# Optimization experiments

Hardware: AMD Instinct MI355X
Metric: run time of the kernel (lower is better)

The kernel has to match this reference:

```python
import jax, jax.numpy as jnp
import numpy as np

NUM_HEADS = 16

def setup_inputs() -> dict:
    B, S, H = 2, 2048, 1024
    Hh = H // 2
    key = jax.random.key(0)
    ks = jax.random.split(key, 16)
    sd = 1.0 / np.sqrt(H)
    sdh = 1.0 / np.sqrt(Hh)
    return {
        "query": jax.random.normal(ks[0], (B, S, H), jnp.float32),
        "key_in": jax.random.normal(ks[1], (B, S, H), jnp.float32),
        "value": jax.random.normal(ks[2], (B, S, H), jnp.float32),
        "direction_signal": jax.random.randint(ks[3], (B, S), 0, 3, jnp.int64),
        # Linear weights stored as (in, out); y = x @ W + b (same math as torch x @ W.T + b)
        "Wq_w": jax.random.normal(ks[4], (H, H), jnp.float32) * sd,
        "Wq_b": jnp.zeros((H,), jnp.float32),
        "Wk_w": jax.random.normal(ks[5], (H, H), jnp.float32) * sd,
        "Wk_b": jnp.zeros((H,), jnp.float32),
        "Wv_w": jax.random.normal(ks[6], (H, H), jnp.float32) * sd,
        "Wv_b": jnp.zeros((H,), jnp.float32),
        "ds1_w": jax.random.normal(ks[7], (H, Hh), jnp.float32) * sd,
        "ds1_b": jnp.zeros((Hh,), jnp.float32),
        "ds2_w": jax.random.normal(ks[8], (Hh, NUM_HEADS), jnp.float32) * sdh,
        "ds2_b": jnp.zeros((NUM_HEADS,), jnp.float32),
        "fo_w": jax.random.normal(ks[9], (H, H), jnp.float32) * sd,
        "fo_b": jnp.zeros((H,), jnp.float32),
    }

def reference(query, key_in, value, direction_signal,
              Wq_w, Wq_b, Wk_w, Wk_b, Wv_w, Wv_b,
              ds1_w, ds1_b, ds2_w, ds2_b, fo_w, fo_b):
    B, S, H = query.shape
    nh = NUM_HEADS
    hd = H // nh
    scale = np.sqrt(hd).astype(np.float32)

    def split_heads(x):  # (B,S,H) -> (B,nh,S,hd)
        return x.reshape(B, S, nh, hd).transpose(0, 2, 1, 3)

    Q = split_heads(query @ Wq_w + Wq_b)
    K = split_heads(key_in @ Wk_w + Wk_b)
    V = split_heads(value @ Wv_w + Wv_b)

    scores = jnp.einsum('bhqd,bhkd->bhqk', Q, K) / scale

    # direction bias: per-(batch, head, query) additive scalar broadcast over keys
    # torch nn.GELU default is exact (erf) -> approximate=False
    dir_w = jax.nn.gelu(query @ ds1_w + ds1_b, approximate=False) @ ds2_w + ds2_b  # (B,S,nh)
    scores = scores + 0.3 * dir_w.transpose(0, 2, 1)[..., None]

    attention = jax.nn.softmax(scores, axis=-1)
    # dropout is identity in eval/reference mode
    context = jnp.einsum('bhqk,bhkd->bqhd', attention, V).reshape(B, S, H)
    output = context @ fo_w + fo_b
    return output, attention
```

## Files before the change

kernel.cpp:

```cpp
#include <hip/hip_runtime.h>


typedef unsigned short u16;
typedef unsigned int   u32;
typedef _Float16       f16;
typedef f16   half8   __attribute__((ext_vector_type(8)));
typedef float floatx4 __attribute__((ext_vector_type(4)));
typedef u32   u32x4   __attribute__((ext_vector_type(4)));

union V8 { u16 u[8]; u32x4 v; };

__device__ __forceinline__ u16 f16_bits(float f){
    union { f16 h; u16 u; } x; x.h = (f16)f; return x.u;
}

template<typename TI>
__global__ __launch_bounds__(256) void transpose_k(
    const TI* __restrict__ in, u16* __restrict__ out,
    long irs, long ors, int zdiv, long ibs0, long ibs1, long obs0, long obs1)
{
    __shared__ u16 tile[64][72];
    int z = blockIdx.z;
    const TI* ip = in  + (long)(z / zdiv) * ibs0 + (long)(z % zdiv) * ibs1;
    u16*      op = out + (long)(z / zdiv) * obs0 + (long)(z % zdiv) * obs1;
    long r0 = (long)blockIdx.y * 64, c0 = (long)blockIdx.x * 64;
    int t = threadIdx.x;
    int r = t >> 2, cs = (t & 3) * 16;
#pragma unroll
    for (int j = 0; j < 16; j++){
        TI v = ip[(r0 + r) * irs + c0 + cs + j];
        if (sizeof(TI) == 4) tile[r][cs + j] = f16_bits((float)v);
        else                 tile[r][cs + j] = (u16)v;
    }
    __syncthreads();
#pragma unroll
    for (int j = 0; j < 16; j++){
        op[(c0 + r) * ors + r0 + cs + j] = tile[cs + j][r];
    }
}

__global__ __launch_bounds__(256) void transpose_w4(
    const float* __restrict__ w0, const float* __restrict__ w1,
    const float* __restrict__ w2, const float* __restrict__ w3,
    u16* __restrict__ o0, u16* __restrict__ o1,
    u16* __restrict__ o2, u16* __restrict__ o3)
{
    __shared__ u16 tile[64][72];
    int z = blockIdx.z;
    const float* ip = (z == 0) ? w0 : (z == 1) ? w1 : (z == 2) ? w2 : w3;
    u16*         op = (z == 0) ? o0 : (z == 1) ? o1 : (z == 2) ? o2 : o3;
    long r0 = (long)blockIdx.y * 64, c0 = (long)blockIdx.x * 64;
    int t = threadIdx.x;
    int r = t >> 2, cs = (t & 3) * 16;
#pragma unroll
    for (int j = 0; j < 16; j++)
        tile[r][cs + j] = f16_bits(ip[(r0 + r) * 1024 + c0 + cs + j]);
    __syncthreads();
#pragma unroll
    for (int j = 0; j < 16; j++)
        op[(c0 + r) * 1024 + r0 + cs + j] = tile[cs + j][r];
}

template<bool A_F32, bool OUT_F32>
__global__ __launch_bounds__(256) void gemm_bt(
    const void* __restrict__ Av, const u16* __restrict__ BT,
    const float* __restrict__ bias, void* __restrict__ Cv,
    int M, int N, int K, float out_scale)
{
    __shared__ u16 Alds[64][40];
    __shared__ u16 Blds[64][40];
    int m0 = blockIdx.y * 64, n0 = blockIdx.x * 64;
    int t = threadIdx.x, w = t >> 6, lane = t & 63, quad = lane >> 4, l16 = lane & 15;
    int wm = (w >> 1) * 32, wn = (w & 1) * 32;
    const floatx4 zero4 = {0.f, 0.f, 0.f, 0.f};
    floatx4 acc[2][2];
#pragma unroll
    for (int i = 0; i < 2; i++)
#pragma unroll
        for (int j = 0; j < 2; j++) acc[i][j] = zero4;

    int srow = t >> 2, scol = (t & 3) * 8;
    const float* Apf = (const float*)Av + (long)(m0 + srow) * K + scol;
    const u16*   Aph = (const u16*)Av   + (long)(m0 + srow) * K + scol;
    const u16*   Bp  = BT + (long)(n0 + srow) * K + scol;

    for (int k0 = 0; k0 < K; k0 += 32){
        __syncthreads();
        V8 va, vb;
        if (A_F32){
            floatx4 a0 = *(const floatx4*)(Apf + k0);
            floatx4 a1 = *(const floatx4*)(Apf + k0 + 4);
#pragma unroll
            for (int j = 0; j < 4; j++){
                va.u[j]     = f16_bits(a0[j]);
                va.u[4 + j] = f16_bits(a1[j]);
            }
        } else {
            va.v = *(const u32x4*)(Aph + k0);
        }
        vb.v = *(const u32x4*)(Bp + k0);
        *(u32x4*)&Alds[srow][scol] = va.v;
        *(u32x4*)&Blds[srow][scol] = vb.v;
        __syncthreads();
        half8 a0 = *(const half8*)&Alds[wm + l16][quad * 8];
        half8 a1 = *(const half8*)&Alds[wm + 16 + l16][quad * 8];
        half8 b0 = *(const half8*)&Blds[wn + l16][quad * 8];
        half8 b1 = *(const half8*)&Blds[wn + 16 + l16][quad * 8];
        acc[0][0] = __builtin_amdgcn_mfma_f32_16x16x32_f16(a0, b0, acc[0][0], 0, 0, 0);
        acc[0][1] = __builtin_amdgcn_mfma_f32_16x16x32_f16(a0, b1, acc[0][1], 0, 0, 0);
        acc[1][0] = __builtin_amdgcn_mfma_f32_16x16x32_f16(a1, b0, acc[1][0], 0, 0, 0);
        acc[1][1] = __builtin_amdgcn_mfma_f32_16x16x32_f16(a1, b1, acc[1][1], 0, 0, 0);
    }

#pragma unroll
    for (int mi = 0; mi < 2; mi++)
#pragma unroll
        for (int ni = 0; ni < 2; ni++){
            int n = n0 + wn + ni * 16 + l16;
            float bv = bias[n];
#pragma unroll
            for (int r = 0; r < 4; r++){
                int m = m0 + wm + mi * 16 + quad * 4 + r;
                float v = (acc[mi][ni][r] + bv) * out_scale;
                if (OUT_F32) ((float*)Cv)[(long)m * N + n] = v;
                else         ((u16*)Cv)[(long)m * N + n]   = f16_bits(v);
            }
        }
}

__global__ __launch_bounds__(256) void gemm_qkv(
    const float* __restrict__ Aq, const float* __restrict__ Ak, const float* __restrict__ Avv,
    const u16* __restrict__ Bq, const u16* __restrict__ Bk, const u16* __restrict__ Bv,
    const float* __restrict__ bq, const float* __restrict__ bk, const float* __restrict__ bv,
    u16* __restrict__ Cq, u16* __restrict__ Ck, u16* __restrict__ Cv,
    int M, int N, int K)
{
    __shared__ u16 Alds[64][40];
    __shared__ u16 Blds[64][40];
    int z = blockIdx.z;
    const float* A    = (z == 0) ? Aq : (z == 1) ? Ak : Avv;
    const u16*   BT   = (z == 0) ? Bq : (z == 1) ? Bk : Bv;
    const float* bias = (z == 0) ? bq : (z == 1) ? bk : bv;
    u16*         C    = (z == 0) ? Cq : (z == 1) ? Ck : Cv;
    float out_scale   = (z == 0) ? 0.125f : 1.0f;

    int m0 = blockIdx.y * 64, n0 = blockIdx.x * 64;
    int t = threadIdx.x, w = t >> 6, lane = t & 63, quad = lane >> 4, l16 = lane & 15;
    int wm = (w >> 1) * 32, wn = (w & 1) * 32;
    const floatx4 zero4 = {0.f, 0.f, 0.f, 0.f};
    floatx4 acc[2][2];
#pragma unroll
    for (int i = 0; i < 2; i++)
#pragma unroll
        for (int j = 0; j < 2; j++) acc[i][j] = zero4;

    int srow = t >> 2, scol = (t & 3) * 8;
    const float* Apf = A + (long)(m0 + srow) * K + scol;
    const u16*   Bp  = BT + (long)(n0 + srow) * K + scol;

    for (int k0 = 0; k0 < K; k0 += 32){
        __syncthreads();
        V8 va, vb;
        floatx4 a0 = *(const floatx4*)(Apf + k0);
        floatx4 a1 = *(const floatx4*)(Apf + k0 + 4);
#pragma unroll
        for (int j = 0; j < 4; j++){
            va.u[j]     = f16_bits(a0[j]);
            va.u[4 + j] = f16_bits(a1[j]);
        }
        vb.v = *(const u32x4*)(Bp + k0);
        *(u32x4*)&Alds[srow][scol] = va.v;
        *(u32x4*)&Blds[srow][scol] = vb.v;
        __syncthreads();
        half8 af0 = *(const half8*)&Alds[wm + l16][quad * 8];
        half8 af1 = *(const half8*)&Alds[wm + 16 + l16][quad * 8];
        half8 bf0 = *(const half8*)&Blds[wn + l16][quad * 8];
        half8 bf1 = *(const half8*)&Blds[wn + 16 + l16][quad * 8];
        acc[0][0] = __builtin_amdgcn_mfma_f32_16x16x32_f16(af0, bf0, acc[0][0], 0, 0, 0);
        acc[0][1] = __builtin_amdgcn_mfma_f32_16x16x32_f16(af0, bf1, acc[0][1], 0, 0, 0);
        acc[1][0] = __builtin_amdgcn_mfma_f32_16x16x32_f16(af1, bf0, acc[1][0], 0, 0, 0);
        acc[1][1] = __builtin_amdgcn_mfma_f32_16x16x32_f16(af1, bf1, acc[1][1], 0, 0, 0);
    }

#pragma unroll
    for (int mi = 0; mi < 2; mi++)
#pragma unroll
        for (int ni = 0; ni < 2; ni++){
            int n = n0 + wn + ni * 16 + l16;
            float bv = bias[n];
#pragma unroll
            for (int r = 0; r < 4; r++){
                int m = m0 + wm + mi * 16 + quad * 4 + r;
                C[(long)m * N + n] = f16_bits((acc[mi][ni][r] + bv) * out_scale);
            }
        }
}

#define S_LEN 2048
#define NH 16
#define HD 64

__global__ __launch_bounds__(256, 4) void attn_k(
    const u16* __restrict__ Q, const u16* __restrict__ K,
    const u16* __restrict__ VT, float* __restrict__ attn,
    u16* __restrict__ ctx)
{
    __shared__ u16 Plds[64][72];
    int bx0 = blockIdx.x;
    int bx = ((bx0 & 7) << 7) | (bx0 >> 3);
    int qb = bx & 31, h = (bx >> 5) & 15, b = bx >> 9;
    int q0 = qb * 64;
    int t = threadIdx.x, w = t >> 6, lane = t & 63, quad = lane >> 4, l16 = lane & 15;
    const u16* Qp  = Q + (long)b * S_LEN * 1024 + h * HD;
    const u16* Kp  = K + (long)b * S_LEN * 1024 + h * HD;
    const u16* VTp = VT + ((long)(b * NH + h)) * HD * S_LEN;

    int qrow = q0 + w * 16 + l16;
    half8 qf0 = *(const half8*)(Qp + (long)qrow * 1024 + quad * 8);
    half8 qf1 = *(const half8*)(Qp + (long)qrow * 1024 + 32 + quad * 8);

    const floatx4 zero4 = {0.f, 0.f, 0.f, 0.f};
    float lsum[4] = {0.f, 0.f, 0.f, 0.f};

    for (int k0 = 0; k0 < S_LEN; k0 += 64){
        floatx4 sc[4];
#pragma unroll
        for (int kt = 0; kt < 4; kt++){
            const u16* kr = Kp + (long)(k0 + kt * 16 + l16) * 1024;
            half8 kf0 = *(const half8*)(kr + quad * 8);
            half8 kf1 = *(const half8*)(kr + 32 + quad * 8);
            sc[kt] = __builtin_amdgcn_mfma_f32_16x16x32_f16(qf0, kf0, zero4, 0, 0, 0);
            sc[kt] = __builtin_amdgcn_mfma_f32_16x16x32_f16(qf1, kf1, sc[kt], 0, 0, 0);
        }
#pragma unroll
        for (int kt = 0; kt < 4; kt++)
#pragma unroll
            for (int r = 0; r < 4; r++) lsum[r] += __expf(sc[kt][r]);
    }
    float linv[4];
#pragma unroll
    for (int r = 0; r < 4; r++){
        float s = lsum[r];
#pragma unroll
        for (int off = 1; off < 16; off <<= 1) s += __shfl_xor(s, off);
        linv[r] = 1.f / s;
    }

    floatx4 ctxa[4];
#pragma unroll
    for (int dt = 0; dt < 4; dt++) ctxa[dt] = zero4;

    long arow0 = ((long)(b * NH + h) * S_LEN + (q0 + w * 16 + quad * 4)) * S_LEN;

    for (int k0 = 0; k0 < S_LEN; k0 += 64){
        floatx4 sc[4];
#pragma unroll
        for (int kt = 0; kt < 4; kt++){
            const u16* kr = Kp + (long)(k0 + kt * 16 + l16) * 1024;
            half8 kf0 = *(const half8*)(kr + quad * 8);
            half8 kf1 = *(const half8*)(kr + 32 + quad * 8);
            sc[kt] = __builtin_amdgcn_mfma_f32_16x16x32_f16(qf0, kf0, zero4, 0, 0, 0);
            sc[kt] = __builtin_amdgcn_mfma_f32_16x16x32_f16(qf1, kf1, sc[kt], 0, 0, 0);
        }
#pragma unroll
        for (int kt = 0; kt < 4; kt++)
#pragma unroll
            for (int r = 0; r < 4; r++){
                float p = __expf(sc[kt][r]) * linv[r];
                __builtin_nontemporal_store(p,
                    &attn[arow0 + (long)r * S_LEN + k0 + kt * 16 + l16]);
                Plds[w * 16 + quad * 4 + r][kt * 16 + l16] = f16_bits(p);
            }
#pragma unroll
        for (int kk = 0; kk < 2; kk++){
            half8 pf = *(const half8*)&Plds[w * 16 + l16][kk * 32 + quad * 8];
#pragma unroll
            for (int dt = 0; dt < 4; dt++){
                const u16* vr = VTp + (long)(dt * 16 + l16) * S_LEN + k0 + kk * 32 + quad * 8;
                half8 vf = *(const half8*)vr;
                ctxa[dt] = __builtin_amdgcn_mfma_f32_16x16x32_f16(pf, vf, ctxa[dt], 0, 0, 0);
            }
        }
    }

    __syncthreads();
#pragma unroll
    for (int dt = 0; dt < 4; dt++)
#pragma unroll
        for (int r = 0; r < 4; r++)
            Plds[w * 16 + quad * 4 + r][dt * 16 + l16] = f16_bits(ctxa[dt][r]);
    __syncthreads();
    {
        int srow = t >> 2, sseg = (t & 3) * 16;
        V8 o0, o1;
#pragma unroll
        for (int j = 0; j < 8; j++){
            o0.u[j] = Plds[srow][sseg + j];
            o1.u[j] = Plds[srow][sseg + 8 + j];
        }
        long cbase = ((long)b * S_LEN + q0 + srow) * 1024 + h * HD + sseg;
        *(u32x4*)(ctx + cbase)     = o0.v;
        *(u32x4*)(ctx + cbase + 8) = o1.v;
    }
}

extern "C" void kernel_launch(void* const* d_in, const int* in_sizes, int n_in,
                              void* d_out, int out_size, void* d_ws, size_t ws_size,
                              hipStream_t stream)
{
    (void)in_sizes; (void)n_in; (void)out_size; (void)ws_size;
    const float* query  = (const float*)d_in[0];
    const float* key_in = (const float*)d_in[1];
    const float* value  = (const float*)d_in[2];
    const float* Wq_w = (const float*)d_in[4];  const float* Wq_b = (const float*)d_in[5];
    const float* Wk_w = (const float*)d_in[6];  const float* Wk_b = (const float*)d_in[7];
    const float* Wv_w = (const float*)d_in[8];  const float* Wv_b = (const float*)d_in[9];
    const float* fo_w = (const float*)d_in[14]; const float* fo_b = (const float*)d_in[15];

    float* out  = (float*)d_out;
    float* attn = out + 4194304L;

    u16* ws  = (u16*)d_ws;
    u16* WqT = ws;
    u16* WkT = WqT + 1048576;
    u16* WvT = WkT + 1048576;
    u16* foT = WvT + 1048576;
    u16* Qm  = foT + 1048576;
    u16* Km  = Qm  + 4194304;
    u16* Vm  = Km  + 4194304;
    u16* VTm = Vm  + 4194304;
    u16* CTX = VTm + 4194304;

    dim3 blk(256);
    transpose_w4<<<dim3(16,16,4), blk, 0, stream>>>(
        Wq_w, Wk_w, Wv_w, fo_w, WqT, WkT, WvT, foT);
    gemm_qkv<<<dim3(16,64,3), blk, 0, stream>>>(
        query, key_in, value, WqT, WkT, WvT, Wq_b, Wk_b, Wv_b,
        Qm, Km, Vm, 4096, 1024, 1024);
    transpose_k<u16><<<dim3(1,32,32), blk, 0, stream>>>(Vm, VTm, 1024, 2048, 16,
        2048L*1024, 64, 16L*64*2048, 64L*2048);
    attn_k<<<dim3(1024), blk, 0, stream>>>(Qm, Km, VTm, attn, CTX);
    gemm_bt<false,true><<<dim3(16,64), blk, 0, stream>>>(CTX, foT, fo_b, out, 4096,1024,1024, 1.0f);
}
```

Measured before the change: 970.5 us.

## Stage K/V tiles in LDS and process two query tiles per attention block

Each attention block now handles 128 query rows (two 64-row tiles) instead of 64, and the grid is halved. K and V tiles are loaded cooperatively into shared memory with a register prefetch of the next tile, so each K/V fetch is reused across both query tiles and all waves instead of every wave reading global memory directly. The MFMA operands are swapped so each lane holds four consecutive key columns, which lets the probability matrix be written with 16-byte non-temporal vector stores. The cost is more LDS, extra barriers per tile and higher register pressure, with the occupancy hint dropped from the launch bounds.

```diff
diff --git a/kernel.cpp b/kernel.cpp
--- a/kernel.cpp
+++ b/kernel.cpp
@@ -200,107 +200,167 @@
 #define NH 16
 #define HD 64
 
-__global__ __launch_bounds__(256, 4) void attn_k(
+__global__ __launch_bounds__(256) void attn_k(
     const u16* __restrict__ Q, const u16* __restrict__ K,
     const u16* __restrict__ VT, float* __restrict__ attn,
     u16* __restrict__ ctx)
 {
-    __shared__ u16 Plds[64][72];
+    __shared__ u16 Klds[64][72];
+    __shared__ u16 Vlds[64][72];
+    __shared__ u16 P0  [64][72];
+    __shared__ u16 P1  [64][72];
+
     int bx0 = blockIdx.x;
-    int bx = ((bx0 & 7) << 7) | (bx0 >> 3);
-    int qb = bx & 31, h = (bx >> 5) & 15, b = bx >> 9;
-    int q0 = qb * 64;
+    int bx = ((bx0 & 7) << 6) | (bx0 >> 3);
+    int qb = bx & 15, h = (bx >> 4) & 15, b = bx >> 8;
+    int qbase = qb * 128;
     int t = threadIdx.x, w = t >> 6, lane = t & 63, quad = lane >> 4, l16 = lane & 15;
     const u16* Qp  = Q + (long)b * S_LEN * 1024 + h * HD;
     const u16* Kp  = K + (long)b * S_LEN * 1024 + h * HD;
     const u16* VTp = VT + ((long)(b * NH + h)) * HD * S_LEN;
 
-    int qrow = q0 + w * 16 + l16;
-    half8 qf0 = *(const half8*)(Qp + (long)qrow * 1024 + quad * 8);
-    half8 qf1 = *(const half8*)(Qp + (long)qrow * 1024 + 32 + quad * 8);
+    const u16* q0p = Qp + (long)(qbase + w * 16 + l16) * 1024;
+    const u16* q1p = q0p + 64 * 1024;
+    half8 qa0 = *(const half8*)(q0p + quad * 8);
+    half8 qa1 = *(const half8*)(q0p + 32 + quad * 8);
+    half8 qb0 = *(const half8*)(q1p + quad * 8);
+    half8 qb1 = *(const half8*)(q1p + 32 + quad * 8);
 
     const floatx4 zero4 = {0.f, 0.f, 0.f, 0.f};
-    float lsum[4] = {0.f, 0.f, 0.f, 0.f};
-
-    for (int k0 = 0; k0 < S_LEN; k0 += 64){
-        floatx4 sc[4];
-#pragma unroll
-        for (int kt = 0; kt < 4; kt++){
-            const u16* kr = Kp + (long)(k0 + kt * 16 + l16) * 1024;
-            half8 kf0 = *(const half8*)(kr + quad * 8);
-            half8 kf1 = *(const half8*)(kr + 32 + quad * 8);
-            sc[kt] = __builtin_amdgcn_mfma_f32_16x16x32_f16(qf0, kf0, zero4, 0, 0, 0);
-            sc[kt] = __builtin_amdgcn_mfma_f32_16x16x32_f16(qf1, kf1, sc[kt], 0, 0, 0);
-        }
-#pragma unroll
-        for (int kt = 0; kt < 4; kt++)
-#pragma unroll
-            for (int r = 0; r < 4; r++) lsum[r] += __expf(sc[kt][r]);
-    }
-    float linv[4];
-#pragma unroll
-    for (int r = 0; r < 4; r++){
-        float s = lsum[r];
-#pragma unroll
-        for (int off = 1; off < 16; off <<= 1) s += __shfl_xor(s, off);
-        linv[r] = 1.f / s;
-    }
-
-    floatx4 ctxa[4];
-#pragma unroll
-    for (int dt = 0; dt < 4; dt++) ctxa[dt] = zero4;
-
-    long arow0 = ((long)(b * NH + h) * S_LEN + (q0 + w * 16 + quad * 4)) * S_LEN;
-
-    for (int k0 = 0; k0 < S_LEN; k0 += 64){
-        floatx4 sc[4];
-#pragma unroll
-        for (int kt = 0; kt < 4; kt++){
-            const u16* kr = Kp + (long)(k0 + kt * 16 + l16) * 1024;
-            half8 kf0 = *(const half8*)(kr + quad * 8);
-            half8 kf1 = *(const half8*)(kr + 32 + quad * 8);
-            sc[kt] = __builtin_amdgcn_mfma_f32_16x16x32_f16(qf0, kf0, zero4, 0, 0, 0);
-            sc[kt] = __builtin_amdgcn_mfma_f32_16x16x32_f16(qf1, kf1, sc[kt], 0, 0, 0);
-        }
-#pragma unroll
-        for (int kt = 0; kt < 4; kt++)
-#pragma unroll
-            for (int r = 0; r < 4; r++){
-                float p = __expf(sc[kt][r]) * linv[r];
-                __builtin_nontemporal_store(p,
-                    &attn[arow0 + (long)r * S_LEN + k0 + kt * 16 + l16]);
-                Plds[w * 16 + quad * 4 + r][kt * 16 + l16] = f16_bits(p);
-            }
-#pragma unroll
-        for (int kk = 0; kk < 2; kk++){
-            half8 pf = *(const half8*)&Plds[w * 16 + l16][kk * 32 + quad * 8];
-#pragma unroll
-            for (int dt = 0; dt < 4; dt++){
-                const u16* vr = VTp + (long)(dt * 16 + l16) * S_LEN + k0 + kk * 32 + quad * 8;
-                half8 vf = *(const half8*)vr;
-                ctxa[dt] = __builtin_amdgcn_mfma_f32_16x16x32_f16(pf, vf, ctxa[dt], 0, 0, 0);
-            }
-        }
-    }
-
-    __syncthreads();
+    int srow = t >> 2, sseg = (t & 3) * 16;
+
+    const u16* kptr = Kp + (long)srow * 1024 + sseg;
+    const u16* vptr = VTp + (long)srow * S_LEN + sseg;
+
+    float lsum0 = 0.f, lsum1 = 0.f;
+    {
+        u32x4 pk0 = *(const u32x4*)(kptr);
+        u32x4 pk1 = *(const u32x4*)(kptr + 8);
+        const u16* kp = kptr + 64 * 1024;
+        for (int it = 0; it < 32; ++it){
+            __syncthreads();
+            *(u32x4*)&Klds[srow][sseg]     = pk0;
+            *(u32x4*)&Klds[srow][sseg + 8] = pk1;
+            __syncthreads();
+            if (it < 31){
+                pk0 = *(const u32x4*)(kp);
+                pk1 = *(const u32x4*)(kp + 8);
+                kp += 64 * 1024;
+            }
+#pragma unroll
+            for (int kt = 0; kt < 4; kt++){
+                half8 kf0 = *(const half8*)&Klds[kt * 16 + l16][quad * 8];
+                half8 kf1 = *(const half8*)&Klds[kt * 16 + l16][32 + quad * 8];
+                floatx4 s0 = __builtin_amdgcn_mfma_f32_16x16x32_f16(kf0, qa0, zero4, 0, 0, 0);
+                s0 = __builtin_amdgcn_mfma_f32_16x16x32_f16(kf1, qa1, s0, 0, 0, 0);
+                floatx4 s1 = __builtin_amdgcn_mfma_f32_16x16x32_f16(kf0, qb0, zero4, 0, 0, 0);
+                s1 = __builtin_amdgcn_mfma_f32_16x16x32_f16(kf1, qb1, s1, 0, 0, 0);
+#pragma unroll
+                for (int r = 0; r < 4; r++){
+                    lsum0 += __expf(s0[r]);
+                    lsum1 += __expf(s1[r]);
+                }
+            }
+        }
+    }
+    lsum0 += __shfl_xor(lsum0, 16); lsum0 += __shfl_xor(lsum0, 32);
+    lsum1 += __shfl_xor(lsum1, 16); lsum1 += __shfl_xor(lsum1, 32);
+    float linv0 = 1.f / lsum0, linv1 = 1.f / lsum1;
+
+    floatx4 cta[4], ctb[4];
+#pragma unroll
+    for (int dt = 0; dt < 4; dt++){ cta[dt] = zero4; ctb[dt] = zero4; }
+
+    long aq0 = ((long)(b * NH + h) * S_LEN + qbase + w * 16 + l16) * S_LEN;
+    long aq1 = aq0 + 64L * S_LEN;
+
+    {
+        u32x4 pk0 = *(const u32x4*)(kptr);
+        u32x4 pk1 = *(const u32x4*)(kptr + 8);
+        u32x4 pv0 = *(const u32x4*)(vptr);
+        u32x4 pv1 = *(const u32x4*)(vptr + 8);
+        const u16* kp = kptr + 64 * 1024;
+        const u16* vp = vptr + 64;
+        for (int it = 0; it < 32; ++it){
+            int k0 = it * 64;
+            __syncthreads();
+            *(u32x4*)&Klds[srow][sseg]     = pk0;
+            *(u32x4*)&Klds[srow][sseg + 8] = pk1;
+            *(u32x4*)&Vlds[srow][sseg]     = pv0;
+            *(u32x4*)&Vlds[srow][sseg + 8] = pv1;
+            __syncthreads();
+            if (it < 31){
+                pk0 = *(const u32x4*)(kp);
+                pk1 = *(const u32x4*)(kp + 8);
+                pv0 = *(const u32x4*)(vp);
+                pv1 = *(const u32x4*)(vp + 8);
+                kp += 64 * 1024;
+                vp += 64;
+            }
+#pragma unroll
+            for (int kt = 0; kt < 4; kt++){
+                half8 kf0 = *(const half8*)&Klds[kt * 16 + l16][quad * 8];
+                half8 kf1 = *(const half8*)&Klds[kt * 16 + l16][32 + quad * 8];
+                floatx4 s0 = __builtin_amdgcn_mfma_f32_16x16x32_f16(kf0, qa0, zero4, 0, 0, 0);
+                s0 = __builtin_amdgcn_mfma_f32_16x16x32_f16(kf1, qa1, s0, 0, 0, 0);
+                floatx4 s1 = __builtin_amdgcn_mfma_f32_16x16x32_f16(kf0, qb0, zero4, 0, 0, 0);
+                s1 = __builtin_amdgcn_mfma_f32_16x16x32_f16(kf1, qb1, s1, 0, 0, 0);
+                floatx4 p0;
+#pragma unroll
+                for (int r = 0; r < 4; r++) p0[r] = __expf(s0[r]) * linv0;
+                __builtin_nontemporal_store(p0,
+                    (floatx4*)(attn + aq0 + k0 + kt * 16 + quad * 4));
+                u32 pa01 = (u32)f16_bits(p0[0]) | ((u32)f16_bits(p0[1]) << 16);
+                u32 pa23 = (u32)f16_bits(p0[2]) | ((u32)f16_bits(p0[3]) << 16);
+                *(u32*)&P0[w * 16 + l16][kt * 16 + quad * 4]     = pa01;
+                *(u32*)&P0[w * 16 + l16][kt * 16 + quad * 4 + 2] = pa23;
+                floatx4 p1;
+#pragma unroll
+                for (int r = 0; r < 4; r++) p1[r] = __expf(s1[r]) * linv1;
+                __builtin_nontemporal_store(p1,
+                    (floatx4*)(attn + aq1 + k0 + kt * 16 + quad * 4));
+                u32 pb01 = (u32)f16_bits(p1[0]) | ((u32)f16_bits(p1[1]) << 16);
+                u32 pb23 = (u32)f16_bits(p1[2]) | ((u32)f16_bits(p1[3]) << 16);
+                *(u32*)&P1[w * 16 + l16][kt * 16 + quad * 4]     = pb01;
+                *(u32*)&P1[w * 16 + l16][kt * 16 + quad * 4 + 2] = pb23;
+            }
+#pragma unroll
+            for (int kk = 0; kk < 2; kk++){
+                half8 pf0 = *(const half8*)&P0[w * 16 + l16][kk * 32 + quad * 8];
+                half8 pf1 = *(const half8*)&P1[w * 16 + l16][kk * 32 + quad * 8];
+#pragma unroll
+                for (int dt = 0; dt < 4; dt++){
+                    half8 vf = *(const half8*)&Vlds[dt * 16 + l16][kk * 32 + quad * 8];
+                    cta[dt] = __builtin_amdgcn_mfma_f32_16x16x32_f16(vf, pf0, cta[dt], 0, 0, 0);
+                    ctb[dt] = __builtin_amdgcn_mfma_f32_16x16x32_f16(vf, pf1, ctb[dt], 0, 0, 0);
+                }
+            }
+        }
+    }
+
 #pragma unroll
     for (int dt = 0; dt < 4; dt++)
 #pragma unroll
-        for (int r = 0; r < 4; r++)
-            Plds[w * 16 + quad * 4 + r][dt * 16 + l16] = f16_bits(ctxa[dt][r]);
+        for (int r = 0; r < 4; r++){
+            P0[w * 16 + l16][dt * 16 + quad * 4 + r] = f16_bits(cta[dt][r]);
+            P1[w * 16 + l16][dt * 16 + quad * 4 + r] = f16_bits(ctb[dt][r]);
+        }
     __syncthreads();
     {
-        int srow = t >> 2, sseg = (t & 3) * 16;
-        V8 o0, o1;
+        V8 o0, o1, o2, o3;
 #pragma unroll
         for (int j = 0; j < 8; j++){
-            o0.u[j] = Plds[srow][sseg + j];
-            o1.u[j] = Plds[srow][sseg + 8 + j];
-        }
-        long cbase = ((long)b * S_LEN + q0 + srow) * 1024 + h * HD + sseg;
-        *(u32x4*)(ctx + cbase)     = o0.v;
-        *(u32x4*)(ctx + cbase + 8) = o1.v;
+            o0.u[j] = P0[srow][sseg + j];
+            o1.u[j] = P0[srow][sseg + 8 + j];
+            o2.u[j] = P1[srow][sseg + j];
+            o3.u[j] = P1[srow][sseg + 8 + j];
+        }
+        long c0 = ((long)b * S_LEN + qbase + srow) * 1024 + h * HD + sseg;
+        long c1 = c0 + 64L * 1024;
+        *(u32x4*)(ctx + c0)     = o0.v;
+        *(u32x4*)(ctx + c0 + 8) = o1.v;
+        *(u32x4*)(ctx + c1)     = o2.v;
+        *(u32x4*)(ctx + c1 + 8) = o3.v;
     }
 }
 
@@ -339,6 +399,6 @@
         Qm, Km, Vm, 4096, 1024, 1024);
     transpose_k<u16><<<dim3(1,32,32), blk, 0, stream>>>(Vm, VTm, 1024, 2048, 16,
         2048L*1024, 64, 16L*64*2048, 64L*2048);
-    attn_k<<<dim3(1024), blk, 0, stream>>>(Qm, Km, VTm, attn, CTX);
+    attn_k<<<dim3(512), blk, 0, stream>>>(Qm, Km, VTm, attn, CTX);
     gemm_bt<false,true><<<dim3(16,64), blk, 0, stream>>>(CTX, foT, fo_b, out, 4096,1024,1024, 1.0f);
 }
```

Result: faster. 818.5 us (-15.7%).
